# Kernel tuning notes

Hardware: AMD Instinct MI355X
Metric: run time of the kernel (lower is better)

## Reference

```python
import jax, jax.numpy as jnp
import numpy as np

N = 8388608          # total items across all scopes
SEG = 64             # uniform scope (segment) length
TARGET_MAX = 1000000


def setup_inputs() -> dict:
    key = jax.random.key(0)
    k1, k2, k3 = jax.random.split(key, 3)
    mean = jax.random.normal(k1, (N, 1), dtype=jnp.float32)
    variance = jax.random.uniform(k2, (N, 1), dtype=jnp.float32)
    targets = jax.random.randint(k3, (N,), 0, TARGET_MAX, dtype=jnp.int64)
    return {"mean": mean, "variance": variance, "targets": targets, "scope": SEG}


def reference(mean, variance, targets, scope):
    # score = cat(mean, variance) -> column 0 is mean m, column 1 is variance v
    n = mean.shape[0]
    b = n // scope                                   # number of ragged segments (uniform here)
    m = mean[:, 0].reshape(b, scope)
    v = variance[:, 0].reshape(b, scope)
    t = targets.reshape(b, scope)

    # per-segment descending sort by targets
    idx = jnp.argsort(-t, axis=1)                    # [b, scope]
    ms = jnp.take_along_axis(m, idx, axis=1)
    vs = jnp.take_along_axis(v, idx, axis=1)

    # tril(exp(m_i - m_j + (v_i + v_j)/2)).sum(0)[j]
    #   = exp(-m_j + v_j/2) * sum_{i>=j} exp(m_i + v_i/2)
    z = jnp.exp(ms + 0.5 * vs)                       # [b, scope]
    rev_cumsum = jnp.cumsum(z[:, ::-1], axis=1)[:, ::-1]  # sum over i >= j
    logS = -ms + 0.5 * vs + jnp.log(rev_cumsum)      # -log(1/S) = log S

    per_seg_loss = jnp.mean(logS, axis=1)            # torch.mean over the segment
    avg = jnp.sum(per_seg_loss) / b                  # losses / len(scope)
    return avg.reshape(1)                            # matches torch.Tensor([0]) accumulator shape
```

## Files before the change

kernel.cpp:

```cpp
#include <hip/hip_runtime.h>

#define N_TOTAL 8388608
#define SEG 64
#define NSEG (N_TOTAL / SEG)
#define NPAIR (NSEG / 2)
#define TPB 256
#define BLOCKS 2048
#define WAVES (BLOCKS * TPB / 64)
#define ITERS (NPAIR / WAVES)

template <int CTRL>
__device__ __forceinline__ unsigned dpp_qp(unsigned v) {
    return (unsigned)__builtin_amdgcn_update_dpp(0, (int)v, CTRL, 0xf, 0xf, true);
}
template <int CTRL, int ROW_MASK>
__device__ __forceinline__ float dpp_add(float x) {
    int mv = __builtin_amdgcn_update_dpp(0, __float_as_int(x), CTRL, ROW_MASK, 0xf, true);
    return x + __int_as_float(mv);
}
template <int D>
__device__ __forceinline__ unsigned lane_xor_c(unsigned v) {
    if (D == 1) return dpp_qp<0xB1>(v);
    if (D == 2) return dpp_qp<0x4E>(v);
    return (unsigned)__builtin_amdgcn_ds_swizzle((int)v, (D << 10) | 0x1F);
}

__global__ __launch_bounds__(TPB, 8) void mledis_seg2(
    const float2* __restrict__ mean2,
    const float2* __restrict__ var2,
    const int2*   __restrict__ tgt2,
    float* __restrict__ partial)
{
    const int lane = threadIdx.x & 63;
    const int h    = lane >> 5;
    const int l5   = lane & 31;
    const int waveId = blockIdx.x * (TPB / 64) + (threadIdx.x >> 6);

    float2 mc = mean2[waveId * 64 + lane];
    float2 vc = var2 [waveId * 64 + lane];
    int2   tc = tgt2 [waveId * 64 + lane];

    float acc = 0.0f;

    #pragma unroll
    for (int it = 0; it < ITERS; ++it) {
        float2 mn_, vn_; int2 tn_;
        if (it + 1 < ITERS) {
            const int b = (waveId + (it + 1) * WAVES) * 64 + lane;
            mn_ = mean2[b]; vn_ = var2[b]; tn_ = tgt2[b];
        }

        const float z0 = __expf(fmaf(0.5f, vc.x, mc.x));
        const float z1 = __expf(fmaf(0.5f, vc.y, mc.y));
        acc += fmaf(0.5f, vc.x, -mc.x) + fmaf(0.5f, vc.y, -mc.y);

        const unsigned e0 = 2u * (unsigned)l5;
        unsigned k0 = (((unsigned)tc.x) << 6) | (63u - e0);
        unsigned k1 = (((unsigned)tc.y) << 6) | (63u - (e0 + 1u));

        #define CMP_XLANE(K, D)                                              \
            {                                                                \
                const unsigned o0 = lane_xor_c<D>(k0);                       \
                const unsigned o1 = lane_xor_c<D>(k1);                       \
                const bool lower = (l5 & (D)) == 0;                          \
                const bool up    = (l5 & ((K) >> 1)) == 0;                   \
                const bool sel   = (up == lower);                            \
                const unsigned mn0 = min(k0, o0), mx0 = max(k0, o0);         \
                const unsigned mn1 = min(k1, o1), mx1 = max(k1, o1);         \
                k0 = sel ? mn0 : mx0;                                        \
                k1 = sel ? mn1 : mx1;                                        \
            }
        #define CMP_LOCAL(K)                                                 \
            {                                                                \
                const bool up = (l5 & ((K) >> 1)) == 0;                      \
                const unsigned mn = min(k0, k1), mx = max(k0, k1);           \
                k0 = up ? mn : mx;                                           \
                k1 = up ? mx : mn;                                           \
            }
        CMP_LOCAL(2)
        CMP_XLANE(4, 1)  CMP_LOCAL(4)
        CMP_XLANE(8, 2)  CMP_XLANE(8, 1)  CMP_LOCAL(8)
        CMP_XLANE(16, 4) CMP_XLANE(16, 2) CMP_XLANE(16, 1) CMP_LOCAL(16)
        CMP_XLANE(32, 8) CMP_XLANE(32, 4) CMP_XLANE(32, 2) CMP_XLANE(32, 1) CMP_LOCAL(32)
        CMP_XLANE(64, 16) CMP_XLANE(64, 8) CMP_XLANE(64, 4) CMP_XLANE(64, 2) CMP_XLANE(64, 1) CMP_LOCAL(64)
        #undef CMP_XLANE
        #undef CMP_LOCAL

        const int o0i = 63 - (int)(k0 & 63u);
        const int o1i = 63 - (int)(k1 & 63u);
        const int a0 = (h * 32 + (o0i >> 1)) << 2;
        const int a1 = (h * 32 + (o1i >> 1)) << 2;
        const int zi0 = __float_as_int(z0);
        const int zi1 = __float_as_int(z1);
        const float g00 = __int_as_float(__builtin_amdgcn_ds_bpermute(a0, zi0));
        const float g01 = __int_as_float(__builtin_amdgcn_ds_bpermute(a0, zi1));
        const float g10 = __int_as_float(__builtin_amdgcn_ds_bpermute(a1, zi0));
        const float g11 = __int_as_float(__builtin_amdgcn_ds_bpermute(a1, zi1));
        const float za0 = (o0i & 1) ? g01 : g00;
        const float za1 = (o1i & 1) ? g11 : g10;

        float P = za0 + za1;
        P = dpp_add<0x111, 0xf>(P);
        P = dpp_add<0x112, 0xf>(P);
        P = dpp_add<0x114, 0xf>(P);
        P = dpp_add<0x118, 0xf>(P);
        P = dpp_add<0x142, 0xa>(P);
        acc += __logf(P * (P - za1));

        mc = mn_; vc = vn_; tc = tn_;
    }

    #pragma unroll
    for (int off = 32; off > 0; off >>= 1)
        acc += __shfl_xor(acc, off, 64);

    __shared__ float sacc[TPB / 64];
    const int waveInBlock = threadIdx.x >> 6;
    if (lane == 0) sacc[waveInBlock] = acc;
    __syncthreads();
    if (threadIdx.x == 0) {
        float b = 0.0f;
        #pragma unroll
        for (int i = 0; i < TPB / 64; ++i) b += sacc[i];
        partial[blockIdx.x] = b;
    }
}

__global__ __launch_bounds__(TPB) void mledis_final_reduce(
    const float* __restrict__ partial, float* __restrict__ out)
{
    float s = 0.0f;
    for (int i = threadIdx.x; i < BLOCKS; i += TPB) s += partial[i];
    #pragma unroll
    for (int off = 32; off > 0; off >>= 1) s += __shfl_xor(s, off, 64);

    __shared__ float sacc[TPB / 64];
    const int lane = threadIdx.x & 63;
    const int w = threadIdx.x >> 6;
    if (lane == 0) sacc[w] = s;
    __syncthreads();
    if (threadIdx.x == 0) {
        float tot = 0.0f;
        #pragma unroll
        for (int i = 0; i < TPB / 64; ++i) tot += sacc[i];
        out[0] = tot * (1.0f / (float)N_TOTAL);
    }
}

extern "C" void kernel_launch(void* const* d_in, const int* in_sizes, int n_in,
                              void* d_out, int out_size, void* d_ws, size_t ws_size,
                              hipStream_t stream) {
    const float2* mean2 = (const float2*)d_in[0];
    const float2* var2  = (const float2*)d_in[1];
    const int2*   tgt2  = (const int2*)d_in[2];

    float* partial = (float*)d_ws;
    float* out = (float*)d_out;

    mledis_seg2<<<BLOCKS, TPB, 0, stream>>>(mean2, var2, tgt2, partial);
    mledis_final_reduce<<<1, TPB, 0, stream>>>(partial, out);
}
```

Baseline: 122.1 us.

## Pack z values as fp16 pairs, use DPP for xor-4/8 exchanges, simplify compare-swap

The two z values per lane are packed into one fp16x2 register, so the gather needs two ds_bpermute calls instead of four. The lane-xor exchanges at distances 4 and 8 move from ds_swizzle to DPP row shifts and row_ror, avoiding LDS-path latency. The compare-swap steps are rewritten as a single compare plus selects instead of min/max pairs. The fp16 packing loses precision and can overflow for large exp values, which may change the loss result.

```diff
diff --git a/kernel.cpp b/kernel.cpp
--- a/kernel.cpp
+++ b/kernel.cpp
@@ -9,9 +9,11 @@
 #define WAVES (BLOCKS * TPB / 64)
 #define ITERS (NPAIR / WAVES)
 
-template <int CTRL>
-__device__ __forceinline__ unsigned dpp_qp(unsigned v) {
-    return (unsigned)__builtin_amdgcn_update_dpp(0, (int)v, CTRL, 0xf, 0xf, true);
+typedef __fp16 h2_t __attribute__((ext_vector_type(2)));
+
+template <int CTRL, int RM, int BM, bool BC>
+__device__ __forceinline__ unsigned dpp_mov(unsigned old, unsigned src) {
+    return (unsigned)__builtin_amdgcn_update_dpp((int)old, (int)src, CTRL, RM, BM, BC);
 }
 template <int CTRL, int ROW_MASK>
 __device__ __forceinline__ float dpp_add(float x) {
@@ -20,8 +22,13 @@
 }
 template <int D>
 __device__ __forceinline__ unsigned lane_xor_c(unsigned v) {
-    if (D == 1) return dpp_qp<0xB1>(v);
-    if (D == 2) return dpp_qp<0x4E>(v);
+    if (D == 1) return dpp_mov<0xB1, 0xf, 0xf, true>(0u, v);
+    if (D == 2) return dpp_mov<0x4E, 0xf, 0xf, true>(0u, v);
+    if (D == 4) {
+        unsigned t = dpp_mov<0x114, 0xf, 0xA, false>(0u, v);
+        return dpp_mov<0x104, 0xf, 0x5, false>(t, v);
+    }
+    if (D == 8) return dpp_mov<0x128, 0xf, 0xf, true>(0u, v);
     return (unsigned)__builtin_amdgcn_ds_swizzle((int)v, (D << 10) | 0x1F);
 }
 
@@ -62,20 +69,16 @@
             {                                                                \
                 const unsigned o0 = lane_xor_c<D>(k0);                       \
                 const unsigned o1 = lane_xor_c<D>(k1);                       \
-                const bool lower = (l5 & (D)) == 0;                          \
-                const bool up    = (l5 & ((K) >> 1)) == 0;                   \
-                const bool sel   = (up == lower);                            \
-                const unsigned mn0 = min(k0, o0), mx0 = max(k0, o0);         \
-                const unsigned mn1 = min(k1, o1), mx1 = max(k1, o1);         \
-                k0 = sel ? mn0 : mx0;                                        \
-                k1 = sel ? mn1 : mx1;                                        \
+                const bool sel = ((l5 & (D)) == 0) == ((l5 & ((K) >> 1)) == 0); \
+                k0 = ((k0 < o0) == sel) ? k0 : o0;                           \
+                k1 = ((k1 < o1) == sel) ? k1 : o1;                           \
             }
         #define CMP_LOCAL(K)                                                 \
             {                                                                \
                 const bool up = (l5 & ((K) >> 1)) == 0;                      \
-                const unsigned mn = min(k0, k1), mx = max(k0, k1);           \
-                k0 = up ? mn : mx;                                           \
-                k1 = up ? mx : mn;                                           \
+                const bool c  = (k0 < k1) == up;                             \
+                const unsigned n0 = c ? k0 : k1, n1 = c ? k1 : k0;           \
+                k0 = n0; k1 = n1;                                            \
             }
         CMP_LOCAL(2)
         CMP_XLANE(4, 1)  CMP_LOCAL(4)
@@ -90,14 +93,14 @@
         const int o1i = 63 - (int)(k1 & 63u);
         const int a0 = (h * 32 + (o0i >> 1)) << 2;
         const int a1 = (h * 32 + (o1i >> 1)) << 2;
-        const int zi0 = __float_as_int(z0);
-        const int zi1 = __float_as_int(z1);
-        const float g00 = __int_as_float(__builtin_amdgcn_ds_bpermute(a0, zi0));
-        const float g01 = __int_as_float(__builtin_amdgcn_ds_bpermute(a0, zi1));
-        const float g10 = __int_as_float(__builtin_amdgcn_ds_bpermute(a1, zi0));
-        const float g11 = __int_as_float(__builtin_amdgcn_ds_bpermute(a1, zi1));
-        const float za0 = (o0i & 1) ? g01 : g00;
-        const float za1 = (o1i & 1) ? g11 : g10;
+        const h2_t pk = __builtin_amdgcn_cvt_pkrtz(z0, z1);
+        const int pki = __builtin_bit_cast(int, pk);
+        const int gi0 = __builtin_amdgcn_ds_bpermute(a0, pki);
+        const int gi1 = __builtin_amdgcn_ds_bpermute(a1, pki);
+        const h2_t gh0 = __builtin_bit_cast(h2_t, gi0);
+        const h2_t gh1 = __builtin_bit_cast(h2_t, gi1);
+        const float za0 = (float)((o0i & 1) ? gh0.y : gh0.x);
+        const float za1 = (float)((o1i & 1) ? gh1.y : gh1.x);
 
         float P = za0 + za1;
         P = dpp_add<0x111, 0xf>(P);
```

Result: slower. 125.9 us (+3.1%).
